# Kernel tuning notes

Measured on AMD Instinct MI355X. Metric: run time of the kernel, lower is better.

## Reference

```python
import jax, jax.numpy as jnp
import numpy as np
import math

N = 4096
D = 256


def _xavier(key, shape):
    fan_in, fan_out = shape[0], shape[1]
    std = math.sqrt(2.0 / (fan_in + fan_out))
    return jax.random.normal(key, shape, dtype=jnp.float32) * std


def setup_inputs() -> dict:
    key = jax.random.key(0)
    ks = jax.random.split(key, 12)
    return {
        "cur": jax.random.normal(ks[0], (N, D), dtype=jnp.float32),
        "pre": jax.random.normal(ks[1], (N, D), dtype=jnp.float32),
        # SpatialHyperedge params
        "r_proj_s": _xavier(ks[2], (D, D)),
        "incidence_s": _xavier(ks[3], (N, N - 1)),
        # TemporalHyperedge params
        "r_proj_t": _xavier(ks[4], (D, D)),
        "incidence_t": _xavier(ks[5], (N, N)),
        # HHNodeMP params
        "node_proj": _xavier(ks[6], (D, D)),
        "spa_edge_proj": _xavier(ks[7], (D, D)),
        "tmp_edge_proj": _xavier(ks[8], (D, D)),
        "theta_w": _xavier(ks[9], (D, D)),
        "theta_b": jnp.zeros((D,), dtype=jnp.float32),
    }


def _scatter_slave(vals):
    """Place [N, N-1] per-row slave values into a zero-diagonal [N, N] matrix.
    Row i's k-th slave is column k if k < i else k+1 (all j != i in order)."""
    n = vals.shape[0]
    k = jnp.arange(n - 1)[None, :]
    cols = k + (k >= jnp.arange(n)[:, None])  # [N, N-1] column indices
    rows = jnp.broadcast_to(jnp.arange(n)[:, None], (n, n - 1))
    return jnp.zeros((n, n), dtype=vals.dtype).at[rows.reshape(-1), cols.reshape(-1)].set(vals.reshape(-1))


def _fro(x):
    return jnp.sqrt(jnp.sum(x * x))


def reference(cur, pre, r_proj_s, incidence_s, r_proj_t, incidence_t,
              node_proj, spa_edge_proj, tmp_edge_proj, theta_w, theta_b):
    n, d = cur.shape
    inv_sqrt_d = 1.0 / math.sqrt(d)

    # ---- SpatialHyperedge ----
    Xd = jax.lax.stop_gradient(cur)
    master_s = Xd @ r_proj_s                                   # [N, D]
    M_s_full = _scatter_slave(incidence_s)                     # [N, N], zero diag
    neigh_recon_s = M_s_full @ Xd                              # == bmm over gathered slaves
    spatial_loss = (_fro(master_s - neigh_recon_s) * 0.2
                    + jnp.sum(jnp.abs(incidence_s))
                    + 0.001 * _fro(incidence_s))
    # clamp(min=0) then zero-out entries not strictly > 0  => relu-like
    clipped_s = jnp.where(incidence_s > 0.0, incidence_s, 0.0)
    incidence_all = _scatter_slave(clipped_s) + jnp.eye(n, dtype=cur.dtype)

    # ---- TemporalHyperedge ----
    cur_d = jax.lax.stop_gradient(cur)
    pre_d = jax.lax.stop_gradient(pre)
    master_t = cur_d @ r_proj_t
    neigh_recon_t = incidence_t @ pre_d
    temporal_loss = (_fro(master_t - neigh_recon_t) * 0.2
                     + jnp.sum(jnp.abs(incidence_t))
                     + 0.001 * _fro(incidence_t))
    incidence_t_clipped = jnp.maximum(incidence_t, 0.0)

    # ---- SpatialHyperedgeMP ----
    spa_edge_fea = incidence_all @ cur
    spa_deg = jnp.sum(incidence_all, axis=1, keepdims=True)
    spa_emb = spa_edge_fea / spa_deg                           # [N, D]

    # ---- TemporalHyperedgeMP ----
    tmp_edge_fea = incidence_t_clipped @ pre + cur
    tmp_deg = jnp.sum(incidence_t_clipped, axis=1, keepdims=True) + 1.0
    tmp_emb = tmp_edge_fea / tmp_deg                           # [N, D]

    # ---- HHNodeMP ----
    node_fea = cur @ node_proj
    spa_fea = spa_emb @ spa_edge_proj
    tmp_fea = tmp_emb @ tmp_edge_proj
    spa_attn = jnp.sum(spa_fea * node_fea, axis=1, keepdims=True) * inv_sqrt_d
    tmp_attn = jnp.sum(tmp_fea * node_fea, axis=1, keepdims=True) * inv_sqrt_d
    val = spa_attn * spa_fea + tmp_attn * tmp_fea
    node_emb = jax.nn.relu(val @ theta_w.T + theta_b)          # dropout = identity (eval)

    return node_emb, temporal_loss + spatial_loss
```

## Files before the change

kernel.cpp:

```cpp
#include <hip/hip_runtime.h>
#include <hip/hip_bf16.h>
#include <math.h>

#define NN 4096
#define DD 256

typedef __bf16 bf16x8 __attribute__((ext_vector_type(8)));
typedef short  short8 __attribute__((ext_vector_type(8)));
typedef float  f32x4  __attribute__((ext_vector_type(4)));

#define MFMA16(a, b, c) __builtin_amdgcn_mfma_f32_16x16x32_bf16((a), (b), (c), 0, 0, 0)

__device__ inline bf16x8 brelu(bf16x8 a) {
    short8 s = __builtin_bit_cast(short8, a);
    s = s & ~(s >> 15);
    return __builtin_bit_cast(bf16x8, s);
}

__device__ inline float wave_red(float v) {
#pragma unroll
    for (int o = 32; o > 0; o >>= 1) v += __shfl_down(v, o, 64);
    return v;
}

__device__ inline unsigned short bfbits(float f) {
    return __builtin_bit_cast(unsigned short, (__bf16)f);
}

__global__ __launch_bounds__(256) void k_prep(const float* __restrict__ cur,
                                              const float* __restrict__ pre,
                                              __bf16* __restrict__ cur_bf,
                                              __bf16* __restrict__ curT,
                                              __bf16* __restrict__ preT) {
    const int z = blockIdx.z;
    const int i0 = blockIdx.x * 64, d0 = blockIdx.y * 64;
    const float* src = z ? pre : cur;
    __bf16* dstT = z ? preT : curT;
    __shared__ unsigned short tile[64][72];
    const int t = threadIdx.x;
    const int r = t >> 2, c4 = (t & 3) * 16;
    const float* srow = src + (size_t)(i0 + r) * DD + d0 + c4;
    alignas(16) unsigned short loc[16];
#pragma unroll
    for (int e = 0; e < 4; ++e) {
        float4 v = ((const float4*)srow)[e];
        loc[e * 4 + 0] = bfbits(v.x);
        loc[e * 4 + 1] = bfbits(v.y);
        loc[e * 4 + 2] = bfbits(v.z);
        loc[e * 4 + 3] = bfbits(v.w);
    }
#pragma unroll
    for (int e = 0; e < 16; ++e) tile[r][c4 + e] = loc[e];
    if (z == 0) {
        __bf16* drow = cur_bf + (size_t)(i0 + r) * DD + d0 + c4;
        *(uint4*)drow = *(uint4*)&loc[0];
        *(uint4*)(drow + 8) = *(uint4*)&loc[8];
    }
    __syncthreads();
    alignas(16) unsigned short o[16];
#pragma unroll
    for (int e = 0; e < 16; ++e) o[e] = tile[c4 + e][r];
    __bf16* trow = dstT + (size_t)(d0 + r) * NN + i0 + c4;
    *(uint4*)trow = *(uint4*)&o[0];
    *(uint4*)(trow + 8) = *(uint4*)&o[8];
}

__global__ __launch_bounds__(256) void k_proj(
    const float* __restrict__ a0, const float* __restrict__ a1, const float* __restrict__ a2,
    const float* __restrict__ a3, const float* __restrict__ a4, const float* __restrict__ a5,
    __bf16* __restrict__ o0, __bf16* __restrict__ o1, __bf16* __restrict__ o2,
    __bf16* __restrict__ o3, __bf16* __restrict__ o4, __bf16* __restrict__ o5) {
    const int id = blockIdx.y, r = blockIdx.x, t = threadIdx.x;
    const float* src = id == 0 ? a0 : id == 1 ? a1 : id == 2 ? a2 : id == 3 ? a3 : id == 4 ? a4 : a5;
    __bf16* dst = id == 0 ? o0 : id == 1 ? o1 : id == 2 ? o2 : id == 3 ? o3 : id == 4 ? o4 : o5;
    float v = src[r * DD + t];
    if (id < 5) dst[t * DD + r] = (__bf16)v;
    else        dst[r * DD + t] = (__bf16)v;
}

__global__ __launch_bounds__(256) void k_conv_t(const float* __restrict__ inc,
                                                __bf16* __restrict__ Mbf,
                                                float* __restrict__ rowsum,
                                                float* __restrict__ pAbs, float* __restrict__ pSq) {
    const int i = blockIdx.x, t = threadIdx.x;
    const float4* src = (const float4*)(inc + (size_t)i * NN);
    ushort4* dst = (ushort4*)(Mbf + (size_t)i * NN);
    float rs = 0.f, as = 0.f, qs = 0.f;
#pragma unroll
    for (int e = 0; e < 4; ++e) {
        const int f = t + 256 * e;
        float4 v = src[f];
        float x[4] = {v.x, v.y, v.z, v.w};
        unsigned short o[4];
#pragma unroll
        for (int j = 0; j < 4; ++j) {
            float fv = x[j];
            as += fabsf(fv); qs += fv * fv; rs += fmaxf(fv, 0.f);
            o[j] = bfbits(fv);
        }
        dst[f] = make_ushort4(o[0], o[1], o[2], o[3]);
    }
    __shared__ float red[3][4];
    const int w = t >> 6, lane = t & 63;
    rs = wave_red(rs); as = wave_red(as); qs = wave_red(qs);
    if (lane == 0) { red[0][w] = rs; red[1][w] = as; red[2][w] = qs; }
    __syncthreads();
    if (t == 0) {
        rowsum[i] = red[0][0] + red[0][1] + red[0][2] + red[0][3];
        pAbs[i]   = red[1][0] + red[1][1] + red[1][2] + red[1][3];
        pSq[i]    = red[2][0] + red[2][1] + red[2][2] + red[2][3];
    }
}

__global__ __launch_bounds__(256) void k_conv_s(const float* __restrict__ inc,
                                                __bf16* __restrict__ Mbf,
                                                float* __restrict__ rowsum,
                                                float* __restrict__ pAbs, float* __restrict__ pSq) {
    const int i = blockIdx.x, t = threadIdx.x;
    __shared__ unsigned short row[NN];
    const float* srow = inc + (size_t)i * (NN - 1);
    float rs = 0.f, as = 0.f, qs = 0.f;
#pragma unroll
    for (int e = 0; e < 4; ++e) {
        const int f = t + 256 * e;
        float x[4] = {0.f, 0.f, 0.f, 0.f};
        if (f < 1023) __builtin_memcpy(x, srow + 4 * f, 16);
        else          __builtin_memcpy(x, srow + 4092, 12);
#pragma unroll
        for (int j = 0; j < 4; ++j) {
            const int k = 4 * f + j;
            float fv = x[j];
            as += fabsf(fv); qs += fv * fv; rs += fmaxf(fv, 0.f);
            if (k < NN - 1) row[k + (k >= i)] = bfbits(fv);
        }
    }
    if (t == 0) row[i] = 0;
    __syncthreads();
    uint4* dOut = (uint4*)(Mbf + (size_t)i * NN);
    const uint4* sIn = (const uint4*)row;
    dOut[t] = sIn[t];
    dOut[t + 256] = sIn[t + 256];
    __shared__ float red[3][4];
    const int w = t >> 6, lane = t & 63;
    rs = wave_red(rs); as = wave_red(as); qs = wave_red(qs);
    if (lane == 0) { red[0][w] = rs; red[1][w] = as; red[2][w] = qs; }
    __syncthreads();
    if (t == 0) {
        rowsum[i] = red[0][0] + red[0][1] + red[0][2] + red[0][3];
        pAbs[i]   = red[1][0] + red[1][1] + red[1][2] + red[1][3];
        pSq[i]    = red[2][0] + red[2][1] + red[2][2] + red[2][3];
    }
}

template <int DUAL>
__device__ inline void mfma_step(const __bf16 (&As)[64][72], const __bf16 (&Bs)[64][72],
                                 int wr, int wc, int quad, int l16,
                                 f32x4 (&accR)[2][2], f32x4 (&accL)[2][2]) {
#pragma unroll
    for (int ks = 0; ks < 2; ++ks) {
        const int kc = ks * 32 + quad * 8;
        bf16x8 a0 = *(const bf16x8*)&As[wr * 32 + l16][kc];
        bf16x8 a1 = *(const bf16x8*)&As[wr * 32 + 16 + l16][kc];
        bf16x8 b0 = *(const bf16x8*)&Bs[wc * 32 + l16][kc];
        bf16x8 b1 = *(const bf16x8*)&Bs[wc * 32 + 16 + l16][kc];
        accR[0][0] = MFMA16(a0, b0, accR[0][0]);
        accR[0][1] = MFMA16(a0, b1, accR[0][1]);
        accR[1][0] = MFMA16(a1, b0, accR[1][0]);
        accR[1][1] = MFMA16(a1, b1, accR[1][1]);
        if (DUAL) {
            bf16x8 a0r = brelu(a0), a1r = brelu(a1);
            accL[0][0] = MFMA16(a0r, b0, accL[0][0]);
            accL[0][1] = MFMA16(a0r, b1, accL[0][1]);
            accL[1][0] = MFMA16(a1r, b0, accL[1][0]);
            accL[1][1] = MFMA16(a1r, b1, accL[1][1]);
        }
    }
}

__global__ __launch_bounds__(256) void k_big(const __bf16* __restrict__ Mt, const __bf16* __restrict__ Ms,
                                             const __bf16* __restrict__ preT, const __bf16* __restrict__ curT,
                                             const float* __restrict__ negMt, const float* __restrict__ negMs,
                                             const float* __restrict__ cur,
                                             float* __restrict__ feaT, float* __restrict__ feaS,
                                             float* __restrict__ pDiff) {
    const int z = blockIdx.z;
    const __bf16* A  = z ? Ms : Mt;
    const __bf16* BT = z ? curT : preT;
    const float* negM = z ? negMs : negMt;
    float* fea = z ? feaS : feaT;
    const int n0 = blockIdx.x * 64, m0 = blockIdx.y * 64;
    __shared__ __bf16 As[64][72], Bs[64][72];
    __shared__ float sred[4];
    f32x4 accR[2][2], accL[2][2];
#pragma unroll
    for (int i = 0; i < 2; ++i)
#pragma unroll
        for (int j = 0; j < 2; ++j) { accR[i][j] = (f32x4)0.f; accL[i][j] = (f32x4)0.f; }
    const int t = threadIdx.x, w = t >> 6, lane = t & 63, quad = lane >> 4, l16 = lane & 15;
    const int wr = w >> 1, wc = w & 1;
    const int sr = t >> 2, sc = (t & 3) * 16;
    const __bf16* gA = A + (size_t)(m0 + sr) * NN + sc;
    const __bf16* gB = BT + (size_t)(n0 + sr) * NN + sc;
    for (int kt = 0; kt < NN / 64; ++kt) {
        uint4 av0 = *(const uint4*)(gA);
        uint4 av1 = *(const uint4*)(gA + 8);
        uint4 bv0 = *(const uint4*)(gB);
        uint4 bv1 = *(const uint4*)(gB + 8);
        __syncthreads();
        *(uint4*)&As[sr][sc] = av0; *(uint4*)&As[sr][sc + 8] = av1;
        *(uint4*)&Bs[sr][sc] = bv0; *(uint4*)&Bs[sr][sc + 8] = bv1;
        __syncthreads();
        mfma_step<1>(As, Bs, wr, wc, quad, l16, accR, accL);
        gA += 64; gB += 64;
    }
    float sumd = 0.f;
#pragma unroll
    for (int mi = 0; mi < 2; ++mi)
#pragma unroll
        for (int ni = 0; ni < 2; ++ni)
#pragma unroll
            for (int r = 0; r < 4; ++r) {
                int gr = m0 + wr * 32 + mi * 16 + quad * 4 + r;
                int gc = n0 + wc * 32 + ni * 16 + l16;
                size_t idx = (size_t)gr * DD + gc;
                float diff = accR[mi][ni][r] + negM[idx];
                sumd += diff * diff;
                fea[idx] = accL[mi][ni][r] + cur[idx];
            }
    sumd = wave_red(sumd);
    if (lane == 0) sred[w] = sumd;
    __syncthreads();
    if (t == 0)
        pDiff[z * 256 + blockIdx.y * 4 + blockIdx.x] = sred[0] + sred[1] + sred[2] + sred[3];
}

__global__ __launch_bounds__(256) void k_small3(const __bf16* __restrict__ cur_bf,
                                                const __bf16* __restrict__ pTs, const __bf16* __restrict__ pTt,
                                                const __bf16* __restrict__ pTn,
                                                float* __restrict__ negMs, float* __restrict__ negMt,
                                                float* __restrict__ nodeFea) {
    const int z = blockIdx.z;
    const __bf16* BT = z == 0 ? pTs : (z == 1 ? pTt : pTn);
    const int n0 = blockIdx.x * 64, m0 = blockIdx.y * 64;
    __shared__ __bf16 As[64][72], Bs[64][72];
    f32x4 accR[2][2];
#pragma unroll
    for (int i = 0; i < 2; ++i)
#pragma unroll
        for (int j = 0; j < 2; ++j) accR[i][j] = (f32x4)0.f;
    const int t = threadIdx.x, w = t >> 6, lane = t & 63, quad = lane >> 4, l16 = lane & 15;
    const int wr = w >> 1, wc = w & 1;
    const int sr = t >> 2, sc = (t & 3) * 16;
    const __bf16* gA = cur_bf + (size_t)(m0 + sr) * DD + sc;
    const __bf16* gB = BT + (size_t)(n0 + sr) * DD + sc;
    for (int kt = 0; kt < DD / 64; ++kt) {
        uint4 av0 = *(const uint4*)(gA);
        uint4 av1 = *(const uint4*)(gA + 8);
        uint4 bv0 = *(const uint4*)(gB);
        uint4 bv1 = *(const uint4*)(gB + 8);
        __syncthreads();
        *(uint4*)&As[sr][sc] = av0; *(uint4*)&As[sr][sc + 8] = av1;
        *(uint4*)&Bs[sr][sc] = bv0; *(uint4*)&Bs[sr][sc + 8] = bv1;
        __syncthreads();
        mfma_step<0>(As, Bs, wr, wc, quad, l16, accR, accR);
        gA += 64; gB += 64;
    }
#pragma unroll
    for (int mi = 0; mi < 2; ++mi)
#pragma unroll
        for (int ni = 0; ni < 2; ++ni)
#pragma unroll
            for (int r = 0; r < 4; ++r) {
                int gr = m0 + wr * 32 + mi * 16 + quad * 4 + r;
                int gc = n0 + wc * 32 + ni * 16 + l16;
                size_t idx = (size_t)gr * DD + gc;
                float v = accR[mi][ni][r];
                if (z == 0) negMs[idx] = -v;
                else if (z == 1) negMt[idx] = -v;
                else nodeFea[idx] = v;
            }
}

__global__ __launch_bounds__(256) void k_fea(const float* __restrict__ feaS, const float* __restrict__ feaT,
                                             const float* __restrict__ rsS, const float* __restrict__ rsT,
                                             const __bf16* __restrict__ pTspa, const __bf16* __restrict__ pTtmp,
                                             float* __restrict__ spaF, float* __restrict__ tmpF) {
    const int z = blockIdx.z;
    const float* fea = z ? feaT : feaS;
    const float* rs = z ? rsT : rsS;
    const __bf16* BT = z ? pTtmp : pTspa;
    float* outF = z ? tmpF : spaF;
    const int n0 = blockIdx.x * 64, m0 = blockIdx.y * 64;
    __shared__ __bf16 As[64][72], Bs[64][72];
    f32x4 accR[2][2];
#pragma unroll
    for (int i = 0; i < 2; ++i)
#pragma unroll
        for (int j = 0; j < 2; ++j) accR[i][j] = (f32x4)0.f;
    const int t = threadIdx.x, w = t >> 6, lane = t & 63, quad = lane >> 4, l16 = lane & 15;
    const int wr = w >> 1, wc = w & 1;
    const int sr = t >> 2, sc = (t & 3) * 16;
    const float inv = 1.f / (rs[m0 + sr] + 1.f);
    const float* gA = fea + (size_t)(m0 + sr) * DD + sc;
    const __bf16* gB = BT + (size_t)(n0 + sr) * DD + sc;
    for (int kt = 0; kt < DD / 64; ++kt) {
        __bf16 tmp[16];
#pragma unroll
        for (int e4 = 0; e4 < 4; ++e4) {
            float4 v = ((const float4*)gA)[e4];
            tmp[e4 * 4 + 0] = (__bf16)(v.x * inv);
            tmp[e4 * 4 + 1] = (__bf16)(v.y * inv);
            tmp[e4 * 4 + 2] = (__bf16)(v.z * inv);
            tmp[e4 * 4 + 3] = (__bf16)(v.w * inv);
        }
        uint4 bv0 = *(const uint4*)(gB);
        uint4 bv1 = *(const uint4*)(gB + 8);
        __syncthreads();
        *(uint4*)&As[sr][sc] = *(uint4*)&tmp[0]; *(uint4*)&As[sr][sc + 8] = *(uint4*)&tmp[8];
        *(uint4*)&Bs[sr][sc] = bv0; *(uint4*)&Bs[sr][sc + 8] = bv1;
        __syncthreads();
        mfma_step<0>(As, Bs, wr, wc, quad, l16, accR, accR);
        gA += 64; gB += 64;
    }
#pragma unroll
    for (int mi = 0; mi < 2; ++mi)
#pragma unroll
        for (int ni = 0; ni < 2; ++ni)
#pragma unroll
            for (int r = 0; r < 4; ++r) {
                int gr = m0 + wr * 32 + mi * 16 + quad * 4 + r;
                int gc = n0 + wc * 32 + ni * 16 + l16;
                outF[(size_t)gr * DD + gc] = accR[mi][ni][r];
            }
}

__global__ __launch_bounds__(256) void k_attn(const float* __restrict__ spaF, const float* __restrict__ tmpF,
                                              const float* __restrict__ nodeF,
                                              float* __restrict__ spaA, float* __restrict__ tmpA) {
    const int t = threadIdx.x, w = t >> 6, lane = t & 63;
    const int i = blockIdx.x * 4 + w;
    const float4* sf = (const float4*)(spaF + (size_t)i * DD);
    const float4* tf = (const float4*)(tmpF + (size_t)i * DD);
    const float4* nf = (const float4*)(nodeF + (size_t)i * DD);
    float4 s = sf[lane], p = tf[lane], n = nf[lane];
    float ds = s.x * n.x + s.y * n.y + s.z * n.z + s.w * n.w;
    float dt = p.x * n.x + p.y * n.y + p.z * n.z + p.w * n.w;
    ds = wave_red(ds); dt = wave_red(dt);
    if (lane == 0) { spaA[i] = ds * 0.0625f; tmpA[i] = dt * 0.0625f; }
}

__global__ __launch_bounds__(256) void k_final(const float* __restrict__ spaF, const float* __restrict__ tmpF,
                                               const float* __restrict__ spaA, const float* __restrict__ tmpA,
                                               const __bf16* __restrict__ thetaBf, const float* __restrict__ thetaB,
                                               float* __restrict__ out) {
    const int n0 = blockIdx.x * 64, m0 = blockIdx.y * 64;
    __shared__ __bf16 As[64][72], Bs[64][72];
    f32x4 accR[2][2];
#pragma unroll
    for (int i = 0; i < 2; ++i)
#pragma unroll
        for (int j = 0; j < 2; ++j) accR[i][j] = (f32x4)0.f;
    const int t = threadIdx.x, w = t >> 6, lane = t & 63, quad = lane >> 4, l16 = lane & 15;
    const int wr = w >> 1, wc = w & 1;
    const int sr = t >> 2, sc = (t & 3) * 16;
    const float sa = spaA[m0 + sr], ta = tmpA[m0 + sr];
    const float* gS = spaF + (size_t)(m0 + sr) * DD + sc;
    const float* gT = tmpF + (size_t)(m0 + sr) * DD + sc;
    const __bf16* gB = thetaBf + (size_t)(n0 + sr) * DD + sc;
    for (int kt = 0; kt < DD / 64; ++kt) {
        __bf16 tmp[16];
#pragma unroll
        for (int e4 = 0; e4 < 4; ++e4) {
            float4 vs = ((const float4*)gS)[e4];
            float4 vt = ((const float4*)gT)[e4];
            tmp[e4 * 4 + 0] = (__bf16)(sa * vs.x + ta * vt.x);
            tmp[e4 * 4 + 1] = (__bf16)(sa * vs.y + ta * vt.y);
            tmp[e4 * 4 + 2] = (__bf16)(sa * vs.z + ta * vt.z);
            tmp[e4 * 4 + 3] = (__bf16)(sa * vs.w + ta * vt.w);
        }
        uint4 bv0 = *(const uint4*)(gB);
        uint4 bv1 = *(const uint4*)(gB + 8);
        __syncthreads();
        *(uint4*)&As[sr][sc] = *(uint4*)&tmp[0]; *(uint4*)&As[sr][sc + 8] = *(uint4*)&tmp[8];
        *(uint4*)&Bs[sr][sc] = bv0; *(uint4*)&Bs[sr][sc + 8] = bv1;
        __syncthreads();
        mfma_step<0>(As, Bs, wr, wc, quad, l16, accR, accR);
        gS += 64; gT += 64; gB += 64;
    }
#pragma unroll
    for (int mi = 0; mi < 2; ++mi)
#pragma unroll
        for (int ni = 0; ni < 2; ++ni)
#pragma unroll
            for (int r = 0; r < 4; ++r) {
                int gr = m0 + wr * 32 + mi * 16 + quad * 4 + r;
                int gc = n0 + wc * 32 + ni * 16 + l16;
                float v = accR[mi][ni][r] + thetaB[gc];
                out[(size_t)gr * DD + gc] = fmaxf(v, 0.f);
            }
}

__global__ __launch_bounds__(256) void k_loss(const float* __restrict__ pAbsT, const float* __restrict__ pSqT,
                                              const float* __restrict__ pAbsS, const float* __restrict__ pSqS,
                                              const float* __restrict__ pDiff,
                                              float* __restrict__ out) {
    const int t = threadIdx.x;
    float aT = 0.f, qT = 0.f, aS = 0.f, qS = 0.f;
#pragma unroll
    for (int j = 0; j < 16; ++j) {
        const int i = t + 256 * j;
        aT += pAbsT[i]; qT += pSqT[i]; aS += pAbsS[i]; qS += pSqS[i];
    }
    float dT = pDiff[t], dS = pDiff[256 + t];
    aT = wave_red(aT); qT = wave_red(qT); aS = wave_red(aS); qS = wave_red(qS);
    dT = wave_red(dT); dS = wave_red(dS);
    __shared__ float red[6][4];
    const int w = t >> 6, lane = t & 63;
    if (lane == 0) { red[0][w] = aT; red[1][w] = qT; red[2][w] = aS; red[3][w] = qS; red[4][w] = dT; red[5][w] = dS; }
    __syncthreads();
    if (t == 0) {
        float s[6];
#pragma unroll
        for (int k = 0; k < 6; ++k) s[k] = red[k][0] + red[k][1] + red[k][2] + red[k][3];
        float l = s[0] + 0.001f * sqrtf(s[1]) + 0.2f * sqrtf(s[4])
                + s[2] + 0.001f * sqrtf(s[3]) + 0.2f * sqrtf(s[5]);
        out[(size_t)NN * DD] = l;
    }
}

extern "C" void kernel_launch(void* const* d_in, const int* in_sizes, int n_in,
                              void* d_out, int out_size, void* d_ws, size_t ws_size,
                              hipStream_t stream) {
    (void)in_sizes; (void)n_in; (void)out_size; (void)ws_size;
    const float* cur      = (const float*)d_in[0];
    const float* pre      = (const float*)d_in[1];
    const float* r_proj_s = (const float*)d_in[2];
    const float* inc_s    = (const float*)d_in[3];
    const float* r_proj_t = (const float*)d_in[4];
    const float* inc_t    = (const float*)d_in[5];
    const float* node_pj  = (const float*)d_in[6];
    const float* spa_pj   = (const float*)d_in[7];
    const float* tmp_pj   = (const float*)d_in[8];
    const float* theta_w  = (const float*)d_in[9];
    const float* theta_b  = (const float*)d_in[10];
    float* out = (float*)d_out;

    char* p = (char*)d_ws;
    auto alloc = [&](size_t bytes) -> void* {
        void* r = (void*)p;
        p += (bytes + 255) & ~(size_t)255;
        return r;
    };
    __bf16* Mt      = (__bf16*)alloc((size_t)NN * NN * 2);
    __bf16* Ms      = (__bf16*)alloc((size_t)NN * NN * 2);
    __bf16* cur_bf  = (__bf16*)alloc((size_t)NN * DD * 2);
    __bf16* curT    = (__bf16*)alloc((size_t)NN * DD * 2);
    __bf16* preT    = (__bf16*)alloc((size_t)NN * DD * 2);
    __bf16* pTs     = (__bf16*)alloc((size_t)DD * DD * 2);
    __bf16* pTt     = (__bf16*)alloc((size_t)DD * DD * 2);
    __bf16* pTn     = (__bf16*)alloc((size_t)DD * DD * 2);
    __bf16* pTspa   = (__bf16*)alloc((size_t)DD * DD * 2);
    __bf16* pTtmp   = (__bf16*)alloc((size_t)DD * DD * 2);
    __bf16* thetaBf = (__bf16*)alloc((size_t)DD * DD * 2);
    float* negMs    = (float*)alloc((size_t)NN * DD * 4);
    float* negMt    = (float*)alloc((size_t)NN * DD * 4);
    float* nodeFea  = (float*)alloc((size_t)NN * DD * 4);
    float* feaS     = (float*)alloc((size_t)NN * DD * 4);
    float* feaT     = (float*)alloc((size_t)NN * DD * 4);
    float* spaF     = (float*)alloc((size_t)NN * DD * 4);
    float* tmpF     = (float*)alloc((size_t)NN * DD * 4);
    float* rsS      = (float*)alloc((size_t)NN * 4);
    float* rsT      = (float*)alloc((size_t)NN * 4);
    float* spaA     = (float*)alloc((size_t)NN * 4);
    float* tmpA     = (float*)alloc((size_t)NN * 4);
    float* pAbsT    = (float*)alloc((size_t)NN * 4);
    float* pSqT     = (float*)alloc((size_t)NN * 4);
    float* pAbsS    = (float*)alloc((size_t)NN * 4);
    float* pSqS     = (float*)alloc((size_t)NN * 4);
    float* pDiff    = (float*)alloc(512 * 4);

    k_prep<<<dim3(NN / 64, DD / 64, 2), 256, 0, stream>>>(cur, pre, cur_bf, curT, preT);
    k_proj<<<dim3(DD, 6), 256, 0, stream>>>(r_proj_s, r_proj_t, node_pj, spa_pj, tmp_pj, theta_w,
                                            pTs, pTt, pTn, pTspa, pTtmp, thetaBf);
    k_conv_t<<<NN, 256, 0, stream>>>(inc_t, Mt, rsT, pAbsT, pSqT);
    k_conv_s<<<NN, 256, 0, stream>>>(inc_s, Ms, rsS, pAbsS, pSqS);
    k_small3<<<dim3(4, 64, 3), 256, 0, stream>>>(cur_bf, pTs, pTt, pTn, negMs, negMt, nodeFea);
    k_big<<<dim3(4, 64, 2), 256, 0, stream>>>(Mt, Ms, preT, curT, negMt, negMs, cur, feaT, feaS, pDiff);
    k_fea<<<dim3(4, 64, 2), 256, 0, stream>>>(feaS, feaT, rsS, rsT, pTspa, pTtmp, spaF, tmpF);
    k_attn<<<NN / 4, 256, 0, stream>>>(spaF, tmpF, nodeFea, spaA, tmpA);
    k_final<<<dim3(4, 64), 256, 0, stream>>>(spaF, tmpF, spaA, tmpA, thetaBf, theta_b, out);
    k_loss<<<1, 256, 0, stream>>>(pAbsT, pSqT, pAbsS, pSqS, pDiff, out);
}
```

Measured before the change: 266.1 us.

## Double-buffer big GEMM LDS, swizzle block order, emit normalized bf16 embeddings

The main N×N×D GEMM kernel now uses two LDS buffers with register prefetch, so the global loads for the next tile overlap the MFMA work on the current one. It also raises wave priority around the MFMAs and remaps block indices so that consecutive blocks spread across A row panels. The degree normalization and the bf16 cast move into the GEMM epilogue, which writes bf16 embeddings and halves the intermediate traffic that k_fea reads. The cost is doubled LDS per block, which may lower occupancy, plus hand-placed waitcnt and barrier calls that are correct only if the scheduler keeps them in order.

```diff
diff --git a/kernel.cpp b/kernel.cpp
--- a/kernel.cpp
+++ b/kernel.cpp
@@ -181,15 +181,19 @@
                                              const __bf16* __restrict__ preT, const __bf16* __restrict__ curT,
                                              const float* __restrict__ negMt, const float* __restrict__ negMs,
                                              const float* __restrict__ cur,
-                                             float* __restrict__ feaT, float* __restrict__ feaS,
+                                             const float* __restrict__ rsT, const float* __restrict__ rsS,
+                                             __bf16* __restrict__ embT, __bf16* __restrict__ embS,
                                              float* __restrict__ pDiff) {
-    const int z = blockIdx.z;
+    const int flat = blockIdx.x + 4 * (blockIdx.y + 64 * blockIdx.z);
+    const int swz = (flat & 7) * 64 + (flat >> 3);
+    const int bx = swz & 3, by = (swz >> 2) & 63, z = swz >> 8;
     const __bf16* A  = z ? Ms : Mt;
     const __bf16* BT = z ? curT : preT;
     const float* negM = z ? negMs : negMt;
-    float* fea = z ? feaS : feaT;
-    const int n0 = blockIdx.x * 64, m0 = blockIdx.y * 64;
-    __shared__ __bf16 As[64][72], Bs[64][72];
+    const float* rs   = z ? rsS : rsT;
+    __bf16* emb       = z ? embS : embT;
+    const int n0 = bx * 64, m0 = by * 64;
+    __shared__ __bf16 As[2][64][72], Bs[2][64][72];
     __shared__ float sred[4];
     f32x4 accR[2][2], accL[2][2];
 #pragma unroll
@@ -201,17 +205,41 @@
     const int sr = t >> 2, sc = (t & 3) * 16;
     const __bf16* gA = A + (size_t)(m0 + sr) * NN + sc;
     const __bf16* gB = BT + (size_t)(n0 + sr) * NN + sc;
+    uint4 av0 = *(const uint4*)(gA);
+    uint4 av1 = *(const uint4*)(gA + 8);
+    uint4 bv0 = *(const uint4*)(gB);
+    uint4 bv1 = *(const uint4*)(gB + 8);
+    gA += 64; gB += 64;
+    *(uint4*)&As[0][sr][sc] = av0; *(uint4*)&As[0][sr][sc + 8] = av1;
+    *(uint4*)&Bs[0][sr][sc] = bv0; *(uint4*)&Bs[0][sr][sc + 8] = bv1;
+    av0 = *(const uint4*)(gA);
+    av1 = *(const uint4*)(gA + 8);
+    bv0 = *(const uint4*)(gB);
+    bv1 = *(const uint4*)(gB + 8);
+    gA += 64; gB += 64;
+    __builtin_amdgcn_sched_barrier(0);
+    asm volatile("s_waitcnt lgkmcnt(0)" ::: "memory");
+    __builtin_amdgcn_s_barrier();
+    int c = 0;
     for (int kt = 0; kt < NN / 64; ++kt) {
-        uint4 av0 = *(const uint4*)(gA);
-        uint4 av1 = *(const uint4*)(gA + 8);
-        uint4 bv0 = *(const uint4*)(gB);
-        uint4 bv1 = *(const uint4*)(gB + 8);
-        __syncthreads();
-        *(uint4*)&As[sr][sc] = av0; *(uint4*)&As[sr][sc + 8] = av1;
-        *(uint4*)&Bs[sr][sc] = bv0; *(uint4*)&Bs[sr][sc + 8] = bv1;
-        __syncthreads();
-        mfma_step<1>(As, Bs, wr, wc, quad, l16, accR, accL);
-        gA += 64; gB += 64;
+        __builtin_amdgcn_s_setprio(1);
+        mfma_step<1>(As[c], Bs[c], wr, wc, quad, l16, accR, accL);
+        __builtin_amdgcn_s_setprio(0);
+        if (kt < NN / 64 - 1) {
+            *(uint4*)&As[c ^ 1][sr][sc] = av0; *(uint4*)&As[c ^ 1][sr][sc + 8] = av1;
+            *(uint4*)&Bs[c ^ 1][sr][sc] = bv0; *(uint4*)&Bs[c ^ 1][sr][sc + 8] = bv1;
+            if (kt < NN / 64 - 2) {
+                av0 = *(const uint4*)(gA);
+                av1 = *(const uint4*)(gA + 8);
+                bv0 = *(const uint4*)(gB);
+                bv1 = *(const uint4*)(gB + 8);
+                gA += 64; gB += 64;
+            }
+            __builtin_amdgcn_sched_barrier(0);
+            asm volatile("s_waitcnt lgkmcnt(0)" ::: "memory");
+        }
+        __builtin_amdgcn_s_barrier();
+        c ^= 1;
     }
     float sumd = 0.f;
 #pragma unroll
@@ -225,13 +253,14 @@
                 size_t idx = (size_t)gr * DD + gc;
                 float diff = accR[mi][ni][r] + negM[idx];
                 sumd += diff * diff;
-                fea[idx] = accL[mi][ni][r] + cur[idx];
+                float inv = 1.f / (rs[gr] + 1.f);
+                emb[idx] = (__bf16)((accL[mi][ni][r] + cur[idx]) * inv);
             }
     sumd = wave_red(sumd);
     if (lane == 0) sred[w] = sumd;
     __syncthreads();
     if (t == 0)
-        pDiff[z * 256 + blockIdx.y * 4 + blockIdx.x] = sred[0] + sred[1] + sred[2] + sred[3];
+        pDiff[z * 256 + by * 4 + bx] = sred[0] + sred[1] + sred[2] + sred[3];
 }
 
 __global__ __launch_bounds__(256) void k_small3(const __bf16* __restrict__ cur_bf,
@@ -281,13 +310,11 @@
             }
 }
 
-__global__ __launch_bounds__(256) void k_fea(const float* __restrict__ feaS, const float* __restrict__ feaT,
-                                             const float* __restrict__ rsS, const float* __restrict__ rsT,
+__global__ __launch_bounds__(256) void k_fea(const __bf16* __restrict__ embS, const __bf16* __restrict__ embT,
                                              const __bf16* __restrict__ pTspa, const __bf16* __restrict__ pTtmp,
                                              float* __restrict__ spaF, float* __restrict__ tmpF) {
     const int z = blockIdx.z;
-    const float* fea = z ? feaT : feaS;
-    const float* rs = z ? rsT : rsS;
+    const __bf16* Ae = z ? embT : embS;
     const __bf16* BT = z ? pTtmp : pTspa;
     float* outF = z ? tmpF : spaF;
     const int n0 = blockIdx.x * 64, m0 = blockIdx.y * 64;
@@ -300,23 +327,15 @@
     const int t = threadIdx.x, w = t >> 6, lane = t & 63, quad = lane >> 4, l16 = lane & 15;
     const int wr = w >> 1, wc = w & 1;
     const int sr = t >> 2, sc = (t & 3) * 16;
-    const float inv = 1.f / (rs[m0 + sr] + 1.f);
-    const float* gA = fea + (size_t)(m0 + sr) * DD + sc;
+    const __bf16* gA = Ae + (size_t)(m0 + sr) * DD + sc;
     const __bf16* gB = BT + (size_t)(n0 + sr) * DD + sc;
     for (int kt = 0; kt < DD / 64; ++kt) {
-        __bf16 tmp[16];
-#pragma unroll
-        for (int e4 = 0; e4 < 4; ++e4) {
-            float4 v = ((const float4*)gA)[e4];
-            tmp[e4 * 4 + 0] = (__bf16)(v.x * inv);
-            tmp[e4 * 4 + 1] = (__bf16)(v.y * inv);
-            tmp[e4 * 4 + 2] = (__bf16)(v.z * inv);
-            tmp[e4 * 4 + 3] = (__bf16)(v.w * inv);
-        }
+        uint4 av0 = *(const uint4*)(gA);
+        uint4 av1 = *(const uint4*)(gA + 8);
         uint4 bv0 = *(const uint4*)(gB);
         uint4 bv1 = *(const uint4*)(gB + 8);
         __syncthreads();
-        *(uint4*)&As[sr][sc] = *(uint4*)&tmp[0]; *(uint4*)&As[sr][sc + 8] = *(uint4*)&tmp[8];
+        *(uint4*)&As[sr][sc] = av0; *(uint4*)&As[sr][sc + 8] = av1;
         *(uint4*)&Bs[sr][sc] = bv0; *(uint4*)&Bs[sr][sc + 8] = bv1;
         __syncthreads();
         mfma_step<0>(As, Bs, wr, wc, quad, l16, accR, accR);
@@ -462,11 +481,11 @@
     __bf16* pTspa   = (__bf16*)alloc((size_t)DD * DD * 2);
     __bf16* pTtmp   = (__bf16*)alloc((size_t)DD * DD * 2);
     __bf16* thetaBf = (__bf16*)alloc((size_t)DD * DD * 2);
+    __bf16* embS    = (__bf16*)alloc((size_t)NN * DD * 2);
+    __bf16* embT    = (__bf16*)alloc((size_t)NN * DD * 2);
     float* negMs    = (float*)alloc((size_t)NN * DD * 4);
     float* negMt    = (float*)alloc((size_t)NN * DD * 4);
     float* nodeFea  = (float*)alloc((size_t)NN * DD * 4);
-    float* feaS     = (float*)alloc((size_t)NN * DD * 4);
-    float* feaT     = (float*)alloc((size_t)NN * DD * 4);
     float* spaF     = (float*)alloc((size_t)NN * DD * 4);
     float* tmpF     = (float*)alloc((size_t)NN * DD * 4);
     float* rsS      = (float*)alloc((size_t)NN * 4);
@@ -485,8 +504,9 @@
     k_conv_t<<<NN, 256, 0, stream>>>(inc_t, Mt, rsT, pAbsT, pSqT);
     k_conv_s<<<NN, 256, 0, stream>>>(inc_s, Ms, rsS, pAbsS, pSqS);
     k_small3<<<dim3(4, 64, 3), 256, 0, stream>>>(cur_bf, pTs, pTt, pTn, negMs, negMt, nodeFea);
-    k_big<<<dim3(4, 64, 2), 256, 0, stream>>>(Mt, Ms, preT, curT, negMt, negMs, cur, feaT, feaS, pDiff);
-    k_fea<<<dim3(4, 64, 2), 256, 0, stream>>>(feaS, feaT, rsS, rsT, pTspa, pTtmp, spaF, tmpF);
+    k_big<<<dim3(4, 64, 2), 256, 0, stream>>>(Mt, Ms, preT, curT, negMt, negMs, cur,
+                                              rsT, rsS, embT, embS, pDiff);
+    k_fea<<<dim3(4, 64, 2), 256, 0, stream>>>(embS, embT, pTspa, pTtmp, spaF, tmpF);
     k_attn<<<NN / 4, 256, 0, stream>>>(spaF, tmpF, nodeFea, spaA, tmpA);
     k_final<<<dim3(4, 64), 256, 0, stream>>>(spaF, tmpF, spaA, tmpA, thetaBf, theta_b, out);
     k_loss<<<1, 256, 0, stream>>>(pAbsT, pSqT, pAbsS, pSqS, pDiff, out);
```

Result: no change. 262.2 us (-1.5%).
